# Kernel tuning notes

Hardware: AMD Instinct MI355X
Metric: run time of the kernel (lower is better)

Reference implementation:

```python
import jax, jax.numpy as jnp
import numpy as np

EPS = 0.5      # sinkhorn eps used by assign_batch_sinkhorn
NITERS = 15    # sinkhorn iterations used by assign_batch_sinkhorn


def pairwise_dists(features, centroids):
    # ||f - c|| via the expansion ||f||^2 + ||c||^2 - 2 f.c (avoids the
    # [B, nc, D] intermediate the naive broadcast would materialize).
    f2 = jnp.sum(features * features, axis=-1)          # [B]
    c2 = jnp.sum(centroids * centroids, axis=-1)        # [K]
    d2 = f2[:, None] + c2[None, :] - 2.0 * features @ centroids.T  # [B, K]
    return jnp.sqrt(jnp.maximum(d2, 0.0))


def sinkhorn(scores, eps=EPS, niters=NITERS):
    # Faithful to the torch sinkhorn(): Q = exp(scores/eps).T, normalize
    # columns (sum over K), then alternate row/column scalings.
    Q = jnp.exp(scores / eps).T                          # [K, B]
    Q = Q / jnp.sum(Q, axis=0, keepdims=True)
    K, B = Q.shape
    r = jnp.ones((K,), Q.dtype) / K
    c = jnp.ones((B,), Q.dtype) / B

    def body(_, Q):
        Q = Q * (r / jnp.sum(Q, axis=1))[:, None]
        Q = Q * (c / jnp.sum(Q, axis=0))[None, :]
        return Q

    Q = jax.lax.fori_loop(0, niters, body, Q)
    return (Q / jnp.sum(Q, axis=0, keepdims=True)).T     # [B, K]


def setup_inputs() -> dict:
    key = jax.random.key(0)
    kf, kc = jax.random.split(key)
    B, K, D = 16384, 2048, 1000
    # 0.1 scale keeps dists ~O(5) so exp(-dists/eps) stays in fp32 range
    # (unit-randn 1000-dim features give dists ~45 -> exp underflow).
    features = 0.1 * jax.random.normal(kf, (B, D), dtype=jnp.float32)
    centroids = 0.1 * jax.random.normal(kc, (K, D), dtype=jnp.float32)
    return {"features": features, "centroids": centroids}


def reference(features, centroids):
    B, K = features.shape[0], centroids.shape[0]
    dists = pairwise_dists(features, centroids)          # [B, K]

    # assign_batch_sinkhorn (soft assignments computed under no_grad)
    soft = jax.lax.stop_gradient(sinkhorn(-dists))       # [B, K]
    batch_assignments = jnp.argmin(soft, axis=1)         # [B] (as in source)
    soft_counts = jnp.sum(soft, axis=0)                  # [K]
    cluster_loss = jnp.mean(
        jnp.take_along_axis(dists, batch_assignments[:, None], axis=1))

    # the per-element python count loops, as fused scatter-adds
    cluster_counts = jnp.zeros((K,), jnp.int32).at[batch_assignments].add(1)
    raw_assign = jnp.argmin(dists, axis=1)
    raw_counts = jnp.zeros((K,), jnp.int32).at[raw_assign].add(1)

    return cluster_loss, batch_assignments, soft_counts, cluster_counts, raw_counts
```

## Files before the change

### kernel.cpp

```cpp
#include <hip/hip_runtime.h>

typedef __attribute__((ext_vector_type(8))) short bf16x8;
typedef __attribute__((ext_vector_type(8))) unsigned short ushort8_t;
typedef __attribute__((ext_vector_type(4))) float f32x4;

#define NB 16384
#define NK 2048
#define ND 1000
#define KP 1024
#define NCHK 1024

__device__ float  g_dist[(size_t)NB * NK];
__device__ ushort g_E[(size_t)NB * NK];
__device__ ushort g_Fh[(size_t)NB * KP], g_Fl[(size_t)NB * KP];
__device__ ushort g_Ch[(size_t)NK * KP], g_Cl[(size_t)NK * KP];
__device__ float  g_u[NK], g_c2[NK];
__device__ float  g_f2[NB], g_bd[NB];
__device__ float  g_part[(size_t)NCHK * NK];
__device__ int    g_cc[NK], g_rc[NK];

typedef const __attribute__((address_space(1))) void gvoid_t;
typedef __attribute__((address_space(3))) void lvoid_t;

union h16 { ushort u; _Float16 h; };

__device__ __forceinline__ ushort bf16_rne(float x){
    uint u = __float_as_uint(x);
    uint lsb = (u >> 16) & 1u;
    u += 0x7fffu + lsb;
    return (ushort)(u >> 16);
}
__device__ __forceinline__ float bf16_to_f(ushort h){
    return __uint_as_float(((uint)h) << 16);
}

template<int WHICH>
__global__ __launch_bounds__(256) void cn_prep(const float* __restrict__ X){
    ushort* __restrict__ H = WHICH ? g_Ch : g_Fh;
    ushort* __restrict__ L = WHICH ? g_Cl : g_Fl;
    float*  __restrict__ sq = WHICH ? g_c2 : g_f2;
    const int row = blockIdx.x, t = threadIdx.x;
    const int lane = t & 63, wid = t >> 6;
    if (WHICH == 1 && t == 0){ g_cc[row] = 0; g_rc[row] = 0; }
    float4 x = make_float4(0.f,0.f,0.f,0.f);
    if (t < 250) x = *(const float4*)(X + (size_t)row * ND + 4 * t);
    double s = (double)x.x*x.x + (double)x.y*x.y + (double)x.z*x.z + (double)x.w*x.w;
    ushort4 h4, l4;
#pragma unroll
    for (int c = 0; c < 4; ++c){
        float xc = (&x.x)[c];
        ushort h = bf16_rne(xc);
        (&h4.x)[c] = h;
        (&l4.x)[c] = bf16_rne(xc - bf16_to_f(h));
    }
    const int base = (t >> 3) << 5;
    const int grp  = (t >> 1) & 3;
    const int pos  = base + ((grp ^ ((row >> 1) & 3)) << 3) + ((4 * t) & 7);
    *(ushort4*)&H[(size_t)row * KP + pos] = h4;
    *(ushort4*)&L[(size_t)row * KP + pos] = l4;

    __shared__ double pr[4];
    for (int off = 32; off; off >>= 1) s += __shfl_xor(s, off);
    if (lane == 0) pr[wid] = s;
    __syncthreads();
    if (t == 0) sq[row] = (float)(pr[0] + pr[1] + pr[2] + pr[3]);
}

__global__ __launch_bounds__(256) void cn_gemm_dist(){
    __shared__ __attribute__((aligned(16))) ushort Ah[128 * 32];
    __shared__ __attribute__((aligned(16))) ushort Al[128 * 32];
    __shared__ __attribute__((aligned(16))) ushort Bh[128 * 32];
    __shared__ __attribute__((aligned(16))) ushort Bl[128 * 32];

    const int tid = threadIdx.x;
    const int lane = tid & 63, wid = tid >> 6;
    const int wr = wid >> 1, wc = wid & 1;
    const int brow0 = blockIdx.y * 128, bcol0 = blockIdx.x * 128;

    f32x4 acc[4][4];
#pragma unroll
    for (int m = 0; m < 4; ++m)
#pragma unroll
        for (int n = 0; n < 4; ++n) acc[m][n] = (f32x4){0.f,0.f,0.f,0.f};

    const int lrow = lane >> 2;
    const int lcol = (lane & 3) * 8;

    for (int step = 0; step < 32; ++step){
        const int k0 = step * 32;
#pragma unroll
        for (int i = 0; i < 2; ++i){
            const int ch = wid * 2 + i;
            const int ldso = ch * 512;
            const size_t ga = ((size_t)(brow0 + ch * 16 + lrow)) * KP + k0 + lcol;
            const size_t gb = ((size_t)(bcol0 + ch * 16 + lrow)) * KP + k0 + lcol;
            __builtin_amdgcn_global_load_lds((gvoid_t*)(g_Fh + ga), (lvoid_t*)(Ah + ldso), 16, 0, 0);
            __builtin_amdgcn_global_load_lds((gvoid_t*)(g_Fl + ga), (lvoid_t*)(Al + ldso), 16, 0, 0);
            __builtin_amdgcn_global_load_lds((gvoid_t*)(g_Ch + gb), (lvoid_t*)(Bh + ldso), 16, 0, 0);
            __builtin_amdgcn_global_load_lds((gvoid_t*)(g_Cl + gb), (lvoid_t*)(Bl + ldso), 16, 0, 0);
        }
        __syncthreads();

        const int arow = wr * 64 + (lane & 15);
        const int brow = wc * 64 + (lane & 15);
        const int kof  = (((lane >> 4) ^ ((lane >> 1) & 3)) * 8);
        bf16x8 afh[4], afl[4], bfh[4], bfl[4];
#pragma unroll
        for (int m = 0; m < 4; ++m){
            afh[m] = *(const bf16x8*)&Ah[(arow + m * 16) * 32 + kof];
            afl[m] = *(const bf16x8*)&Al[(arow + m * 16) * 32 + kof];
        }
#pragma unroll
        for (int n = 0; n < 4; ++n){
            bfh[n] = *(const bf16x8*)&Bh[(brow + n * 16) * 32 + kof];
            bfl[n] = *(const bf16x8*)&Bl[(brow + n * 16) * 32 + kof];
        }
#pragma unroll
        for (int m = 0; m < 4; ++m)
#pragma unroll
            for (int n = 0; n < 4; ++n){
                acc[m][n] = __builtin_amdgcn_mfma_f32_16x16x32_bf16(afh[m], bfh[n], acc[m][n], 0, 0, 0);
                acc[m][n] = __builtin_amdgcn_mfma_f32_16x16x32_bf16(afh[m], bfl[n], acc[m][n], 0, 0, 0);
                acc[m][n] = __builtin_amdgcn_mfma_f32_16x16x32_bf16(afl[m], bfh[n], acc[m][n], 0, 0, 0);
            }
        __syncthreads();
    }

#pragma unroll
    for (int m = 0; m < 4; ++m){
        int rowb = brow0 + wr * 64 + m * 16 + (lane >> 4) * 4;
#pragma unroll
        for (int n = 0; n < 4; ++n){
            int col = bcol0 + wc * 64 + n * 16 + (lane & 15);
            float c2v = g_c2[col];
#pragma unroll
            for (int j = 0; j < 4; ++j){
                float d2 = g_f2[rowb + j] + c2v - 2.0f * acc[m][n][j];
                float d  = sqrtf(fmaxf(d2, 0.0f));
                size_t idx = (size_t)(rowb + j) * NK + col;
                g_dist[idx] = d;
                h16 cv; cv.h = (_Float16)(__expf(-2.0f * d) * 8192.0f);
                g_E[idx] = cv.u;
            }
        }
    }
}

template<int MODE>
__global__ __launch_bounds__(256) void cn_sweep(float* __restrict__ outba){
    __shared__ float4 sred[3][8][64];
    const int lane = threadIdx.x & 63, wid = threadIdx.x >> 6;
    const int row0 = (blockIdx.x * 4 + wid) * 4;
    const float cst = (MODE == 0) ? 1.0f : (1.0f / (float)NB);

    float4 uu[8];
    float4 ak[8];
    if (MODE == 1){
#pragma unroll
        for (int j = 0; j < 4; ++j)
#pragma unroll
            for (int h = 0; h < 2; ++h)
                uu[2 * j + h] = *(const float4*)&g_u[512 * j + 8 * lane + 4 * h];
    }
    if (MODE >= 2){
#pragma unroll
        for (int j = 0; j < 8; ++j)
            uu[j] = *(const float4*)&g_u[4 * lane + 256 * j];
    }
    if (MODE == 3){
#pragma unroll
        for (int j = 0; j < 8; ++j)
#pragma unroll
            for (int c = 0; c < 4; ++c)
                (&ak[j].x)[c] = (float)log((double)(&uu[j].x)[c] * (double)NK);
    }

    float4 S[8];
#pragma unroll
    for (int j = 0; j < 8; ++j) S[j] = make_float4(0.f,0.f,0.f,0.f);

    for (int r = 0; r < 4; ++r){
        const int b = row0 + r;
        float tsum = 0.f;
        if (MODE <= 1){
            ushort8_t q8[4];
            const ushort* er = g_E + (size_t)b * NK + 8 * lane;
#pragma unroll
            for (int j = 0; j < 4; ++j){
                q8[j] = *(const ushort8_t*)(er + 512 * j);
#pragma unroll
                for (int c = 0; c < 8; ++c){
                    h16 cv; cv.u = q8[j][c];
                    float e = (float)cv.h;
                    tsum += (MODE == 1) ? e * (&uu[2 * j + (c >> 2)].x)[c & 3] : e;
                }
            }
#pragma unroll
            for (int off = 32; off; off >>= 1) tsum += __shfl_xor(tsum, off);
            const float v = cst / tsum;
#pragma unroll
            for (int j = 0; j < 4; ++j)
#pragma unroll
                for (int c = 0; c < 8; ++c){
                    h16 cv; cv.u = q8[j][c];
                    (&S[2 * j + (c >> 2)].x)[c & 3] += (float)cv.h * v;
                }
        } else {
            float4 ev[8], dv[8];
            const float* dr = g_dist + (size_t)b * NK + 4 * lane;
#pragma unroll
            for (int j = 0; j < 8; ++j){
                float4 d4 = *(const float4*)(dr + 256 * j);
#pragma unroll
                for (int c = 0; c < 4; ++c){
                    float e = __expf(-2.0f * (&d4.x)[c]);
                    (&ev[j].x)[c] = e;
                    tsum += e * (&uu[j].x)[c];
                }
                if (MODE == 3) dv[j] = d4;
            }
#pragma unroll
            for (int off = 32; off; off >>= 1) tsum += __shfl_xor(tsum, off);
            const float v = cst / tsum;
#pragma unroll
            for (int j = 0; j < 8; ++j){
                S[j].x += ev[j].x * v; S[j].y += ev[j].y * v;
                S[j].z += ev[j].z * v; S[j].w += ev[j].w * v;
            }

            if (MODE == 3){
                double bestT = -1.0e300; int bi = 0; float bd = 0.f;
                float rbest = 3.4e38f;   int ri = 0;
#pragma unroll
                for (int j = 0; j < 8; ++j){
#pragma unroll
                    for (int c = 0; c < 4; ++c){
                        int k = 256 * j + 4 * lane + c;
                        float d = (&dv[j].x)[c];
                        double t = 2.0 * (double)d - (double)(&ak[j].x)[c];
                        if (t > bestT){ bestT = t; bi = k; bd = d; }
                        if (d < rbest){ rbest = d; ri = k; }
                    }
                }
                for (int off = 32; off; off >>= 1){
                    double oT = __shfl_xor(bestT, off);
                    int    oi = __shfl_xor(bi, off);
                    float  od = __shfl_xor(bd, off);
                    if (oT > bestT || (oT == bestT && oi < bi)){ bestT = oT; bi = oi; bd = od; }
                    float orb = __shfl_xor(rbest, off);
                    int   ori = __shfl_xor(ri, off);
                    if (orb < rbest || (orb == rbest && ori < ri)){ rbest = orb; ri = ori; }
                }
                if (lane == 0){
                    outba[b] = (float)bi;
                    g_bd[b] = bd;
                    atomicAdd(&g_cc[bi], 1);
                    atomicAdd(&g_rc[ri], 1);
                }
            }
        }
    }

    if (wid > 0){
#pragma unroll
        for (int j = 0; j < 8; ++j) sred[wid - 1][j][lane] = S[j];
    }
    __syncthreads();
    if (wid == 0){
#pragma unroll
        for (int w = 0; w < 3; ++w)
#pragma unroll
            for (int j = 0; j < 8; ++j){
                float4 o = sred[w][j][lane];
                S[j].x += o.x; S[j].y += o.y; S[j].z += o.z; S[j].w += o.w;
            }
        if (MODE <= 1){
#pragma unroll
            for (int j = 0; j < 4; ++j)
#pragma unroll
                for (int h = 0; h < 2; ++h)
                    *(float4*)&g_part[(size_t)blockIdx.x * NK + 512 * j + 8 * lane + 4 * h] = S[2 * j + h];
        } else {
#pragma unroll
            for (int j = 0; j < 8; ++j)
                *(float4*)&g_part[(size_t)blockIdx.x * NK + 4 * lane + 256 * j] = S[j];
        }
    }
}

__global__ __launch_bounds__(256) void cn_red0(){
    const int sub = threadIdx.x & 31;
    const int k = blockIdx.x * 8 + (threadIdx.x >> 5);
    double s = 0.0;
#pragma unroll 8
    for (int i = 0; i < 32; ++i)
        s += (double)g_part[(size_t)(i * 32 + sub) * NK + k];
    s += __shfl_xor(s, 16); s += __shfl_xor(s, 8);
    s += __shfl_xor(s, 4);  s += __shfl_xor(s, 2);  s += __shfl_xor(s, 1);
    if (sub == 0) g_u[k] = (float)((1.0 / (double)NK) / s);
}

__global__ __launch_bounds__(256) void cn_fin(float* __restrict__ out){
    __shared__ double red[4][64];
    __shared__ double lred[4];
    const int lane = threadIdx.x & 63, q = threadIdx.x >> 6;
    const int k = blockIdx.x * 64 + lane;
    double s = 0.0;
    for (int ch = q * 256; ch < q * 256 + 256; ++ch)
        s += (double)g_part[(size_t)ch * NK + k];
    red[q][lane] = s;
    __syncthreads();
    if (q == 0){
        double tot = red[0][lane] + red[1][lane] + red[2][lane] + red[3][lane];
        out[1 + NB + k] = (float)((double)NB * (double)g_u[k] * tot);
    } else if (q == 1){
        out[1 + NB + NK + k] = (float)g_cc[k];
    } else if (q == 2){
        out[1 + NB + 2 * NK + k] = (float)g_rc[k];
    }
    if (blockIdx.x == 0){
        double sl = 0.0;
        for (int b = threadIdx.x; b < NB; b += 256) sl += (double)g_bd[b];
        for (int off = 32; off; off >>= 1) sl += __shfl_xor(sl, off);
        if (lane == 0) lred[q] = sl;
        __syncthreads();
        if (threadIdx.x == 0)
            out[0] = (float)((lred[0] + lred[1] + lred[2] + lred[3]) / (double)NB);
    }
}

extern "C" void kernel_launch(void* const* d_in, const int* in_sizes, int n_in,
                              void* d_out, int out_size, void* d_ws, size_t ws_size,
                              hipStream_t stream){
    const float* F  = (const float*)d_in[0];
    const float* Cn = (const float*)d_in[1];
    float* out = (float*)d_out;
    (void)d_ws; (void)ws_size;

    cn_prep<0><<<NB, 256, 0, stream>>>(F);
    cn_prep<1><<<NK, 256, 0, stream>>>(Cn);

    dim3 gg(NK / 128, NB / 128);
    cn_gemm_dist<<<gg, 256, 0, stream>>>();

    cn_sweep<0><<<NCHK, 256, 0, stream>>>(nullptr);
    cn_red0<<<NK / 8, 256, 0, stream>>>();
    for (int it = 1; it <= 11; ++it){
        cn_sweep<1><<<NCHK, 256, 0, stream>>>(nullptr);
        cn_red0<<<NK / 8, 256, 0, stream>>>();
    }
    for (int it = 12; it <= 14; ++it){
        cn_sweep<2><<<NCHK, 256, 0, stream>>>(nullptr);
        cn_red0<<<NK / 8, 256, 0, stream>>>();
    }
    cn_sweep<3><<<NCHK, 256, 0, stream>>>(out + 1);
    cn_fin<<<NK / 64, 256, 0, stream>>>(out);
}
```

Measured before the change: 762.1 us.

## Replace fp32 distance matrix with fp16 hi/lo exp-score pair, derive argmins from scores

Drops the fp32 distance matrix. The GEMM epilogue now writes the exp score as two fp16 halves (high part plus residual), and the late Sinkhorn sweeps read those 4 bytes per entry instead of recomputing exp from fp32 distances. The final argmin and raw-argmin are taken on score times column scaling and on max score, and the chosen distance is recovered with a log. The change also merges the two prep launches into one and restructures the column reduction so it uses an LDS cross-wave reduction with better coalescing. The risks are precision loss in the split fp16 representation, possible argmin tie flips, and underflow of small exp values.

```diff
diff --git a/kernel.cpp b/kernel.cpp
--- a/kernel.cpp
+++ b/kernel.cpp
@@ -10,8 +10,8 @@
 #define KP 1024
 #define NCHK 1024
 
-__device__ float  g_dist[(size_t)NB * NK];
 __device__ ushort g_E[(size_t)NB * NK];
+__device__ ushort g_R[(size_t)NB * NK];
 __device__ ushort g_Fh[(size_t)NB * KP], g_Fl[(size_t)NB * KP];
 __device__ ushort g_Ch[(size_t)NK * KP], g_Cl[(size_t)NK * KP];
 __device__ float  g_u[NK], g_c2[NK];
@@ -34,14 +34,17 @@
     return __uint_as_float(((uint)h) << 16);
 }
 
-template<int WHICH>
-__global__ __launch_bounds__(256) void cn_prep(const float* __restrict__ X){
-    ushort* __restrict__ H = WHICH ? g_Ch : g_Fh;
-    ushort* __restrict__ L = WHICH ? g_Cl : g_Fl;
-    float*  __restrict__ sq = WHICH ? g_c2 : g_f2;
-    const int row = blockIdx.x, t = threadIdx.x;
+__global__ __launch_bounds__(256) void cn_prep(const float* __restrict__ F,
+                                               const float* __restrict__ Cn){
+    const int isC = (blockIdx.x >= NB);
+    const int row = isC ? (blockIdx.x - NB) : blockIdx.x;
+    const float* __restrict__ X = isC ? Cn : F;
+    ushort* __restrict__ H = isC ? g_Ch : g_Fh;
+    ushort* __restrict__ L = isC ? g_Cl : g_Fl;
+    float*  __restrict__ sq = isC ? g_c2 : g_f2;
+    const int t = threadIdx.x;
     const int lane = t & 63, wid = t >> 6;
-    if (WHICH == 1 && t == 0){ g_cc[row] = 0; g_rc[row] = 0; }
+    if (isC && t == 0){ g_cc[row] = 0; g_rc[row] = 0; }
     float4 x = make_float4(0.f,0.f,0.f,0.f);
     if (t < 250) x = *(const float4*)(X + (size_t)row * ND + 4 * t);
     double s = (double)x.x*x.x + (double)x.y*x.y + (double)x.z*x.z + (double)x.w*x.w;
@@ -137,10 +140,13 @@
             for (int j = 0; j < 4; ++j){
                 float d2 = g_f2[rowb + j] + c2v - 2.0f * acc[m][n][j];
                 float d  = sqrtf(fmaxf(d2, 0.0f));
+                float e32 = __expf(-2.0f * d) * 8192.0f;
                 size_t idx = (size_t)(rowb + j) * NK + col;
-                g_dist[idx] = d;
-                h16 cv; cv.h = (_Float16)(__expf(-2.0f * d) * 8192.0f);
-                g_E[idx] = cv.u;
+                h16 hv; hv.h = (_Float16)e32;
+                float hf = (float)hv.h;
+                h16 rv; rv.h = (_Float16)(e32 - hf);
+                g_E[idx] = hv.u;
+                g_R[idx] = rv.u;
             }
         }
     }
@@ -154,25 +160,12 @@
     const float cst = (MODE == 0) ? 1.0f : (1.0f / (float)NB);
 
     float4 uu[8];
-    float4 ak[8];
-    if (MODE == 1){
+    if (MODE >= 1){
 #pragma unroll
         for (int j = 0; j < 4; ++j)
 #pragma unroll
             for (int h = 0; h < 2; ++h)
                 uu[2 * j + h] = *(const float4*)&g_u[512 * j + 8 * lane + 4 * h];
-    }
-    if (MODE >= 2){
-#pragma unroll
-        for (int j = 0; j < 8; ++j)
-            uu[j] = *(const float4*)&g_u[4 * lane + 256 * j];
-    }
-    if (MODE == 3){
-#pragma unroll
-        for (int j = 0; j < 8; ++j)
-#pragma unroll
-            for (int c = 0; c < 4; ++c)
-                (&ak[j].x)[c] = (float)log((double)(&uu[j].x)[c] * (double)NK);
     }
 
     float4 S[8];
@@ -206,54 +199,57 @@
                     (&S[2 * j + (c >> 2)].x)[c & 3] += (float)cv.h * v;
                 }
         } else {
-            float4 ev[8], dv[8];
-            const float* dr = g_dist + (size_t)b * NK + 4 * lane;
-#pragma unroll
-            for (int j = 0; j < 8; ++j){
-                float4 d4 = *(const float4*)(dr + 256 * j);
-#pragma unroll
-                for (int c = 0; c < 4; ++c){
-                    float e = __expf(-2.0f * (&d4.x)[c]);
-                    (&ev[j].x)[c] = e;
-                    tsum += e * (&uu[j].x)[c];
-                }
-                if (MODE == 3) dv[j] = d4;
+            float ev[4][8];
+            const ushort* er = g_E + (size_t)b * NK + 8 * lane;
+            const ushort* rr = g_R + (size_t)b * NK + 8 * lane;
+#pragma unroll
+            for (int j = 0; j < 4; ++j){
+                ushort8_t qe = *(const ushort8_t*)(er + 512 * j);
+                ushort8_t qr = *(const ushort8_t*)(rr + 512 * j);
+#pragma unroll
+                for (int c = 0; c < 8; ++c){
+                    h16 cv; cv.u = qe[c];
+                    h16 rv; rv.u = qr[c];
+                    float e = (float)cv.h + (float)rv.h;
+                    ev[j][c] = e;
+                    tsum += e * (&uu[2 * j + (c >> 2)].x)[c & 3];
+                }
             }
 #pragma unroll
             for (int off = 32; off; off >>= 1) tsum += __shfl_xor(tsum, off);
             const float v = cst / tsum;
 #pragma unroll
-            for (int j = 0; j < 8; ++j){
-                S[j].x += ev[j].x * v; S[j].y += ev[j].y * v;
-                S[j].z += ev[j].z * v; S[j].w += ev[j].w * v;
-            }
+            for (int j = 0; j < 4; ++j)
+#pragma unroll
+                for (int c = 0; c < 8; ++c)
+                    (&S[2 * j + (c >> 2)].x)[c & 3] += ev[j][c] * v;
 
             if (MODE == 3){
-                double bestT = -1.0e300; int bi = 0; float bd = 0.f;
-                float rbest = 3.4e38f;   int ri = 0;
-#pragma unroll
-                for (int j = 0; j < 8; ++j){
-#pragma unroll
-                    for (int c = 0; c < 4; ++c){
-                        int k = 256 * j + 4 * lane + c;
-                        float d = (&dv[j].x)[c];
-                        double t = 2.0 * (double)d - (double)(&ak[j].x)[c];
-                        if (t > bestT){ bestT = t; bi = k; bd = d; }
-                        if (d < rbest){ rbest = d; ri = k; }
+                double bestW = 1.0e300; int bi = 0; float be = 1.f;
+                float rbe = -1.f;      int ri = 0;
+#pragma unroll
+                for (int j = 0; j < 4; ++j){
+#pragma unroll
+                    for (int c = 0; c < 8; ++c){
+                        int k = 512 * j + 8 * lane + c;
+                        float e = ev[j][c];
+                        double w = (double)e * (double)(&uu[2 * j + (c >> 2)].x)[c & 3];
+                        if (w < bestW){ bestW = w; bi = k; be = e; }
+                        if (e > rbe){ rbe = e; ri = k; }
                     }
                 }
                 for (int off = 32; off; off >>= 1){
-                    double oT = __shfl_xor(bestT, off);
+                    double oW = __shfl_xor(bestW, off);
                     int    oi = __shfl_xor(bi, off);
-                    float  od = __shfl_xor(bd, off);
-                    if (oT > bestT || (oT == bestT && oi < bi)){ bestT = oT; bi = oi; bd = od; }
-                    float orb = __shfl_xor(rbest, off);
+                    float  oe = __shfl_xor(be, off);
+                    if (oW < bestW || (oW == bestW && oi < bi)){ bestW = oW; bi = oi; be = oe; }
+                    float ore = __shfl_xor(rbe, off);
                     int   ori = __shfl_xor(ri, off);
-                    if (orb < rbest || (orb == rbest && ori < ri)){ rbest = orb; ri = ori; }
+                    if (ore > rbe || (ore == rbe && ori < ri)){ rbe = ore; ri = ori; }
                 }
                 if (lane == 0){
                     outba[b] = (float)bi;
-                    g_bd[b] = bd;
+                    g_bd[b] = (float)(-0.5 * (log((double)be) - 9.010913347279288));
                     atomicAdd(&g_cc[bi], 1);
                     atomicAdd(&g_rc[ri], 1);
                 }
@@ -274,30 +270,31 @@
                 float4 o = sred[w][j][lane];
                 S[j].x += o.x; S[j].y += o.y; S[j].z += o.z; S[j].w += o.w;
             }
-        if (MODE <= 1){
-#pragma unroll
-            for (int j = 0; j < 4; ++j)
-#pragma unroll
-                for (int h = 0; h < 2; ++h)
-                    *(float4*)&g_part[(size_t)blockIdx.x * NK + 512 * j + 8 * lane + 4 * h] = S[2 * j + h];
-        } else {
-#pragma unroll
-            for (int j = 0; j < 8; ++j)
-                *(float4*)&g_part[(size_t)blockIdx.x * NK + 4 * lane + 256 * j] = S[j];
-        }
+#pragma unroll
+        for (int j = 0; j < 4; ++j)
+#pragma unroll
+            for (int h = 0; h < 2; ++h)
+                *(float4*)&g_part[(size_t)blockIdx.x * NK + 512 * j + 8 * lane + 4 * h] = S[2 * j + h];
     }
 }
 
 __global__ __launch_bounds__(256) void cn_red0(){
-    const int sub = threadIdx.x & 31;
-    const int k = blockIdx.x * 8 + (threadIdx.x >> 5);
+    __shared__ double red[4][8];
+    const int kk  = threadIdx.x & 7;
+    const int sub = threadIdx.x >> 3;
+    const int wv  = threadIdx.x >> 6;
+    const int k = blockIdx.x * 8 + kk;
     double s = 0.0;
 #pragma unroll 8
     for (int i = 0; i < 32; ++i)
         s += (double)g_part[(size_t)(i * 32 + sub) * NK + k];
-    s += __shfl_xor(s, 16); s += __shfl_xor(s, 8);
-    s += __shfl_xor(s, 4);  s += __shfl_xor(s, 2);  s += __shfl_xor(s, 1);
-    if (sub == 0) g_u[k] = (float)((1.0 / (double)NK) / s);
+    s += __shfl_xor(s, 8); s += __shfl_xor(s, 16); s += __shfl_xor(s, 32);
+    if ((threadIdx.x & 63) < 8) red[wv][kk] = s;
+    __syncthreads();
+    if (threadIdx.x < 8){
+        double tot = red[0][kk] + red[1][kk] + red[2][kk] + red[3][kk];
+        g_u[blockIdx.x * 8 + kk] = (float)((1.0 / (double)NK) / tot);
+    }
 }
 
 __global__ __launch_bounds__(256) void cn_fin(float* __restrict__ out){
@@ -337,8 +334,7 @@
     float* out = (float*)d_out;
     (void)d_ws; (void)ws_size;
 
-    cn_prep<0><<<NB, 256, 0, stream>>>(F);
-    cn_prep<1><<<NK, 256, 0, stream>>>(Cn);
+    cn_prep<<<NB + NK, 256, 0, stream>>>(F, Cn);
 
     dim3 gg(NK / 128, NB / 128);
     cn_gemm_dist<<<gg, 256, 0, stream>>>();
```

New measurement: 722.7 us. -5.2%, faster.
